# Performance work log

Hardware: AMD Instinct MI355X
Metric: run time of the kernel (lower is better)

Reference implementation:

```python
import jax, jax.numpy as jnp
import numpy as np

N_NODES = 100000
N_EDGES = 3200000

def setup_inputs() -> dict:
    key = jax.random.key(0)
    ks = jax.random.split(key, 13)
    d_in, d1, d2, fm_dims, n_cls = 512, 256, 128, 64, 64
    sc = lambda d: 1.0 / np.sqrt(d)
    return {
        'x': jax.random.normal(ks[0], (N_NODES, d_in), jnp.float32),
        'edge_val': jax.random.uniform(ks[1], (N_EDGES,), jnp.float32),
        'W0': jax.random.normal(ks[2], (d_in, d1), jnp.float32) * sc(d_in),
        'W1': jax.random.normal(ks[3], (d1, d2), jnp.float32) * sc(d1),
        'v0_0': jax.random.normal(ks[4], (d1, 1), jnp.float32) * sc(d1),
        'v0_1': jax.random.normal(ks[5], (d1, 1), jnp.float32) * sc(d1),
        'v1_0': jax.random.normal(ks[6], (d2, 1), jnp.float32) * sc(d2),
        'v1_1': jax.random.normal(ks[7], (d2, 1), jnp.float32) * sc(d2),
        'fm_emb': jax.random.normal(ks[8], (d_in, fm_dims), jnp.float32) * sc(d_in),
        'proj_W': jax.random.normal(ks[9], (d2 + fm_dims, n_cls), jnp.float32) * sc(d2 + fm_dims),
        'proj_b': jnp.zeros((n_cls,), jnp.float32),
        'edge_src': jax.random.randint(ks[10], (N_EDGES,), 0, N_NODES, jnp.int32),
        'edge_dst': jax.random.randint(ks[11], (N_EDGES,), 0, N_NODES, jnp.int32),
    }


def gat_layer(H, W, va, vb, src, dst, a_val, n_nodes):
    # H: [N, d_in] -> Hw: [N, d_out]
    Hw = H @ W
    f1 = (Hw @ va)[:, 0]  # [N]
    f2 = (Hw @ vb)[:, 0]  # [N]
    # per-edge logit: A_ij * f1_i + A_ij * f2_j  (tf sparse broadcast mul + sparse_add)
    logits = a_val * (f1[src] + f2[dst])  # [E]
    s = jax.nn.sigmoid(logits)
    # sparse row softmax over outgoing edges of each src node (stable)
    m = jax.ops.segment_max(s, src, num_segments=n_nodes)  # [N]
    e = jnp.exp(s - m[src])
    denom = jax.ops.segment_sum(e, src, num_segments=n_nodes)  # [N]
    att = e / denom[src]  # [E]
    # aggregate: out[i] = sum_j att_ij * Hw[j]
    out = jax.ops.segment_sum(att[:, None] * Hw[dst], src, num_segments=n_nodes)
    return out


def reference(x, edge_val, W0, W1, v0_0, v0_1, v1_0, v1_1, fm_emb, proj_W, proj_b, edge_src, edge_dst):
    n = x.shape[0]
    # two stacked GAT encoder layers (dropout = 0 at inference)
    H = gat_layer(x, W0, v0_0, v0_1, edge_src, edge_dst, edge_val, n)
    H = gat_layer(H, W1, v1_0, v1_1, edge_src, edge_dst, edge_val, n)
    # NFM bilinear pooling: 0.5 * ((x E)^2 - x (E*E))
    summed = x @ fm_emb
    sq_sum = x @ jnp.square(fm_emb)
    nfm = 0.5 * (jnp.square(summed) - sq_sum)
    # projection to logits
    return jnp.concatenate([H, nfm], axis=1) @ proj_W + proj_b
```

## Files before the change

kernel.cpp:

```cpp
#include <hip/hip_runtime.h>


__device__ __forceinline__ int wave_prefix_incl(int v) {
  int lane = threadIdx.x & 63;
#pragma unroll
  for (int d = 1; d < 64; d <<= 1) {
    int n = __shfl_up(v, d);
    if (lane >= d) v += n;
  }
  return v;
}

__device__ __forceinline__ unsigned short f2bf(float f) {
  unsigned int x = __float_as_uint(f);
  x += 0x7fffu + ((x >> 16) & 1u);
  return (unsigned short)(x >> 16);
}


__global__ void k_hist(const int* __restrict__ src, int* __restrict__ cnt, int E) {
  int e = blockIdx.x * blockDim.x + threadIdx.x;
  if (e < E) atomicAdd(&cnt[src[e]], 1);
}

__global__ void k_scan1(const int* __restrict__ cnt, int* __restrict__ row_ptr,
                        int* __restrict__ partials, int N) {
  int t = threadIdx.x;
  int base = blockIdx.x * 512 + t * 2;
  int e0 = (base < N) ? cnt[base] : 0;
  int e1 = (base + 1 < N) ? cnt[base + 1] : 0;
  int v = e0 + e1;
  int lane = t & 63, wid = t >> 6;
  int incl = wave_prefix_incl(v);
  __shared__ int wsum[4];
  if (lane == 63) wsum[wid] = incl;
  __syncthreads();
  int off = 0;
#pragma unroll
  for (int i = 0; i < 4; ++i)
    if (i < wid) off += wsum[i];
  incl += off;
  int excl = incl - v;
  if (base < N) row_ptr[base] = excl;
  if (base + 1 < N) row_ptr[base + 1] = excl + e0;
  if (t == 255) partials[blockIdx.x] = incl;
}

__global__ void k_scan2(int* partials, int P) {
  int t = threadIdx.x;
  int v = (t < P) ? partials[t] : 0;
  int lane = t & 63, wid = t >> 6;
  int incl = wave_prefix_incl(v);
  __shared__ int wsum[4];
  if (lane == 63) wsum[wid] = incl;
  __syncthreads();
  int off = 0;
#pragma unroll
  for (int i = 0; i < 4; ++i)
    if (i < wid) off += wsum[i];
  incl += off;
  if (t < P) partials[t] = incl - v;
}

__global__ void k_scan3(int* __restrict__ row_ptr, int* __restrict__ cursor,
                        const int* __restrict__ partials, int N, int E) {
  int i = blockIdx.x * blockDim.x + threadIdx.x;
  if (i < N) {
    int v = row_ptr[i] + partials[i >> 9];
    row_ptr[i] = v;
    cursor[i] = v;
  }
  if (i == 0) row_ptr[N] = E;
}

__global__ void k_scatter(const int* __restrict__ src, int* __restrict__ cursor,
                          int* __restrict__ eid, int E) {
  int e = blockIdx.x * blockDim.x + threadIdx.x;
  if (e < E) {
    int p = atomicAdd(&cursor[src[e]], 1);
    eid[p] = e;
  }
}


template <int BM, int BN, int BK>
__global__ __launch_bounds__(256) void k_gemm(const float* __restrict__ A,
                                              const float* __restrict__ B,
                                              float* __restrict__ C, int M, int N,
                                              int K) {
  __shared__ float As[BK][BM];
  __shared__ float Bs[BK][BN];
  int t = threadIdx.x;
  int bm0 = blockIdx.x * BM, bn0 = blockIdx.y * BN;
  int tr = t >> 4, tc = t & 15;
  int row0 = tr * 8, col0 = tc * 4;
  float acc[8][4] = {};
  for (int k0 = 0; k0 < K; k0 += BK) {
#pragma unroll
    for (int i = 0; i < 2; ++i) {
      int s = t + i * 256;
      int ar = s >> 2, akq = (s & 3) * 4;
      int grow = bm0 + ar;
      if (grow >= M) grow = M - 1;
      const float4 av =
          *reinterpret_cast<const float4*>(&A[(size_t)grow * K + k0 + akq]);
      As[akq + 0][ar] = av.x;
      As[akq + 1][ar] = av.y;
      As[akq + 2][ar] = av.z;
      As[akq + 3][ar] = av.w;
    }
    {
      int br = t >> 4, bc = (t & 15) * 4;
      const float4 bv =
          *reinterpret_cast<const float4*>(&B[(size_t)(k0 + br) * N + bn0 + bc]);
      *reinterpret_cast<float4*>(&Bs[br][bc]) = bv;
    }
    __syncthreads();
#pragma unroll
    for (int k = 0; k < BK; ++k) {
      float a0[8], b0[4];
      *reinterpret_cast<float4*>(&a0[0]) =
          *reinterpret_cast<const float4*>(&As[k][row0]);
      *reinterpret_cast<float4*>(&a0[4]) =
          *reinterpret_cast<const float4*>(&As[k][row0 + 4]);
      *reinterpret_cast<float4*>(&b0[0]) =
          *reinterpret_cast<const float4*>(&Bs[k][col0]);
#pragma unroll
      for (int i = 0; i < 8; ++i)
#pragma unroll
        for (int j = 0; j < 4; ++j) acc[i][j] = fmaf(a0[i], b0[j], acc[i][j]);
    }
    __syncthreads();
  }
#pragma unroll
  for (int i = 0; i < 8; ++i) {
    int grow = bm0 + row0 + i;
    if (grow < M) {
      float4 v = {acc[i][0], acc[i][1], acc[i][2], acc[i][3]};
      *reinterpret_cast<float4*>(&C[(size_t)grow * N + bn0 + col0]) = v;
    }
  }
}

template <int BM, int BN, int BK>
__global__ __launch_bounds__(256) void k_gemm_bias(const float* __restrict__ A,
                                                   const float* __restrict__ B,
                                                   const float* __restrict__ bias,
                                                   float* __restrict__ C, int M,
                                                   int N, int K) {
  __shared__ float As[BK][BM];
  __shared__ float Bs[BK][BN];
  int t = threadIdx.x;
  int bm0 = blockIdx.x * BM, bn0 = blockIdx.y * BN;
  int tr = t >> 4, tc = t & 15;
  int row0 = tr * 8, col0 = tc * 4;
  float acc[8][4] = {};
  for (int k0 = 0; k0 < K; k0 += BK) {
#pragma unroll
    for (int i = 0; i < 2; ++i) {
      int s = t + i * 256;
      int ar = s >> 2, akq = (s & 3) * 4;
      int grow = bm0 + ar;
      if (grow >= M) grow = M - 1;
      const float4 av =
          *reinterpret_cast<const float4*>(&A[(size_t)grow * K + k0 + akq]);
      As[akq + 0][ar] = av.x;
      As[akq + 1][ar] = av.y;
      As[akq + 2][ar] = av.z;
      As[akq + 3][ar] = av.w;
    }
    {
      int br = t >> 4, bc = (t & 15) * 4;
      const float4 bv =
          *reinterpret_cast<const float4*>(&B[(size_t)(k0 + br) * N + bn0 + bc]);
      *reinterpret_cast<float4*>(&Bs[br][bc]) = bv;
    }
    __syncthreads();
#pragma unroll
    for (int k = 0; k < BK; ++k) {
      float a0[8], b0[4];
      *reinterpret_cast<float4*>(&a0[0]) =
          *reinterpret_cast<const float4*>(&As[k][row0]);
      *reinterpret_cast<float4*>(&a0[4]) =
          *reinterpret_cast<const float4*>(&As[k][row0 + 4]);
      *reinterpret_cast<float4*>(&b0[0]) =
          *reinterpret_cast<const float4*>(&Bs[k][col0]);
#pragma unroll
      for (int i = 0; i < 8; ++i)
#pragma unroll
        for (int j = 0; j < 4; ++j) acc[i][j] = fmaf(a0[i], b0[j], acc[i][j]);
    }
    __syncthreads();
  }
  const float4 bv = *reinterpret_cast<const float4*>(&bias[bn0 + col0]);
#pragma unroll
  for (int i = 0; i < 8; ++i) {
    int grow = bm0 + row0 + i;
    if (grow < M) {
      float4 v = {acc[i][0] + bv.x, acc[i][1] + bv.y, acc[i][2] + bv.z,
                  acc[i][3] + bv.w};
      *reinterpret_cast<float4*>(&C[(size_t)grow * N + bn0 + col0]) = v;
    }
  }
}

__global__ __launch_bounds__(256) void k_nfm(const float* __restrict__ X,
                                             const float* __restrict__ Emb,
                                             float* __restrict__ out, int M,
                                             int K, int ldo) {
  const int BM = 128, BN = 64, BK = 16;
  __shared__ float As[BK][BM];
  __shared__ float Bs[BK][BN];
  int t = threadIdx.x;
  int bm0 = blockIdx.x * BM;
  int tr = t >> 4, tc = t & 15;
  int row0 = tr * 8, col0 = tc * 4;
  float accS[8][4] = {}, accQ[8][4] = {};
  for (int k0 = 0; k0 < K; k0 += BK) {
#pragma unroll
    for (int i = 0; i < 2; ++i) {
      int s = t + i * 256;
      int ar = s >> 2, akq = (s & 3) * 4;
      int grow = bm0 + ar;
      if (grow >= M) grow = M - 1;
      const float4 av =
          *reinterpret_cast<const float4*>(&X[(size_t)grow * K + k0 + akq]);
      As[akq + 0][ar] = av.x;
      As[akq + 1][ar] = av.y;
      As[akq + 2][ar] = av.z;
      As[akq + 3][ar] = av.w;
    }
    {
      int br = t >> 4, bc = (t & 15) * 4;
      const float4 bv =
          *reinterpret_cast<const float4*>(&Emb[(size_t)(k0 + br) * BN + bc]);
      *reinterpret_cast<float4*>(&Bs[br][bc]) = bv;
    }
    __syncthreads();
#pragma unroll
    for (int k = 0; k < BK; ++k) {
      float a0[8], b0[4], bq[4];
      *reinterpret_cast<float4*>(&a0[0]) =
          *reinterpret_cast<const float4*>(&As[k][row0]);
      *reinterpret_cast<float4*>(&a0[4]) =
          *reinterpret_cast<const float4*>(&As[k][row0 + 4]);
      *reinterpret_cast<float4*>(&b0[0]) =
          *reinterpret_cast<const float4*>(&Bs[k][col0]);
#pragma unroll
      for (int j = 0; j < 4; ++j) bq[j] = b0[j] * b0[j];
#pragma unroll
      for (int i = 0; i < 8; ++i)
#pragma unroll
        for (int j = 0; j < 4; ++j) {
          accS[i][j] = fmaf(a0[i], b0[j], accS[i][j]);
          accQ[i][j] = fmaf(a0[i], bq[j], accQ[i][j]);
        }
    }
    __syncthreads();
  }
#pragma unroll
  for (int i = 0; i < 8; ++i) {
    int grow = bm0 + row0 + i;
    if (grow < M) {
      float4 v;
      v.x = 0.5f * (accS[i][0] * accS[i][0] - accQ[i][0]);
      v.y = 0.5f * (accS[i][1] * accS[i][1] - accQ[i][1]);
      v.z = 0.5f * (accS[i][2] * accS[i][2] - accQ[i][2]);
      v.w = 0.5f * (accS[i][3] * accS[i][3] - accQ[i][3]);
      *reinterpret_cast<float4*>(&out[(size_t)grow * ldo + col0]) = v;
    }
  }
}

__global__ __launch_bounds__(256) void k_cvt_bf16(const float* __restrict__ in,
                                                  unsigned short* __restrict__ out,
                                                  long total) {
  long base = ((long)blockIdx.x * blockDim.x + threadIdx.x) * 8;
  if (base >= total) return;
  float4 a = *reinterpret_cast<const float4*>(&in[base]);
  float4 b = *reinterpret_cast<const float4*>(&in[base + 4]);
  ushort4 lo = {f2bf(a.x), f2bf(a.y), f2bf(a.z), f2bf(a.w)};
  ushort4 hi = {f2bf(b.x), f2bf(b.y), f2bf(b.z), f2bf(b.w)};
  *reinterpret_cast<ushort4*>(&out[base]) = lo;
  *reinterpret_cast<ushort4*>(&out[base + 4]) = hi;
}


template <int D>
__global__ __launch_bounds__(256) void k_fvec(const float* __restrict__ Hw,
                                              const float* __restrict__ va,
                                              const float* __restrict__ vb,
                                              float* __restrict__ f1,
                                              float* __restrict__ f2, int M) {
  int wid = threadIdx.x >> 6, lane = threadIdx.x & 63;
  int i = blockIdx.x * 4 + wid;
  if (i >= M) return;
  const float* row = Hw + (size_t)i * D;
  float s1, s2;
  if (D == 256) {
    float4 h = *reinterpret_cast<const float4*>(&row[lane * 4]);
    float4 a = *reinterpret_cast<const float4*>(&va[lane * 4]);
    float4 b = *reinterpret_cast<const float4*>(&vb[lane * 4]);
    s1 = h.x * a.x + h.y * a.y + h.z * a.z + h.w * a.w;
    s2 = h.x * b.x + h.y * b.y + h.z * b.z + h.w * b.w;
  } else {
    float2 h = *reinterpret_cast<const float2*>(&row[lane * 2]);
    float2 a = *reinterpret_cast<const float2*>(&va[lane * 2]);
    float2 b = *reinterpret_cast<const float2*>(&vb[lane * 2]);
    s1 = h.x * a.x + h.y * a.y;
    s2 = h.x * b.x + h.y * b.y;
  }
#pragma unroll
  for (int d = 32; d; d >>= 1) {
    s1 += __shfl_down(s1, d);
    s2 += __shfl_down(s2, d);
  }
  if (lane == 0) {
    f1[i] = s1;
    f2[i] = s2;
  }
}

__global__ void k_edge(const float* __restrict__ aval, const int* __restrict__ src,
                       const int* __restrict__ dst, const float* __restrict__ f1,
                       const float* __restrict__ f2, float* __restrict__ att,
                       float* __restrict__ denom, int E) {
  int e = blockIdx.x * blockDim.x + threadIdx.x;
  if (e >= E) return;
  float x = aval[e] * (f1[src[e]] + f2[dst[e]]);
  float s = 1.0f / (1.0f + __expf(-x));
  float ev = __expf(s);
  att[e] = ev;
  atomicAdd(&denom[src[e]], ev);
}

template <int D>
__global__ __launch_bounds__(256) void k_agg(const unsigned short* __restrict__ Hwb,
                                             const float* __restrict__ att,
                                             const int* __restrict__ row_ptr,
                                             const int* __restrict__ eid,
                                             const int* __restrict__ dst,
                                             const float* __restrict__ denom,
                                             float* __restrict__ out, int M,
                                             int ldo) {
  int wid = threadIdx.x >> 6, lane = threadIdx.x & 63;
  int i = blockIdx.x * 4 + wid;
  if (i >= M) return;
  int p0 = __builtin_amdgcn_readfirstlane(row_ptr[i]);
  int p1 = __builtin_amdgcn_readfirstlane(row_ptr[i + 1]);
  float acc[8] = {};
  if (D == 256) {
    int half = lane >> 5, q = lane & 31;
    for (int p = p0 + half; p < p1; p += 2) {
      int e = eid[p];
      float w = att[e];
      int j = dst[e];
      uint4 hv =
          *reinterpret_cast<const uint4*>(&Hwb[(size_t)j * 256 + q * 8]);
#pragma unroll
      for (int c = 0; c < 4; ++c) {
        unsigned int u = (&hv.x)[c];
        acc[2 * c + 0] = fmaf(w, __uint_as_float(u << 16), acc[2 * c + 0]);
        acc[2 * c + 1] = fmaf(w, __uint_as_float(u & 0xffff0000u), acc[2 * c + 1]);
      }
    }
#pragma unroll
    for (int c = 0; c < 8; ++c) acc[c] += __shfl_xor(acc[c], 32);
    if (half == 0) {
      float inv = (p1 > p0) ? 1.0f / denom[i] : 0.0f;
      float4 lo = {acc[0] * inv, acc[1] * inv, acc[2] * inv, acc[3] * inv};
      float4 hi = {acc[4] * inv, acc[5] * inv, acc[6] * inv, acc[7] * inv};
      *reinterpret_cast<float4*>(&out[(size_t)i * ldo + q * 8]) = lo;
      *reinterpret_cast<float4*>(&out[(size_t)i * ldo + q * 8 + 4]) = hi;
    }
  } else {
    int quarter = lane >> 4, q = lane & 15;
    for (int p = p0 + quarter; p < p1; p += 4) {
      int e = eid[p];
      float w = att[e];
      int j = dst[e];
      uint4 hv =
          *reinterpret_cast<const uint4*>(&Hwb[(size_t)j * 128 + q * 8]);
#pragma unroll
      for (int c = 0; c < 4; ++c) {
        unsigned int u = (&hv.x)[c];
        acc[2 * c + 0] = fmaf(w, __uint_as_float(u << 16), acc[2 * c + 0]);
        acc[2 * c + 1] = fmaf(w, __uint_as_float(u & 0xffff0000u), acc[2 * c + 1]);
      }
    }
#pragma unroll
    for (int c = 0; c < 8; ++c) acc[c] += __shfl_xor(acc[c], 32);
#pragma unroll
    for (int c = 0; c < 8; ++c) acc[c] += __shfl_xor(acc[c], 16);
    if (quarter == 0) {
      float inv = (p1 > p0) ? 1.0f / denom[i] : 0.0f;
      float4 lo = {acc[0] * inv, acc[1] * inv, acc[2] * inv, acc[3] * inv};
      float4 hi = {acc[4] * inv, acc[5] * inv, acc[6] * inv, acc[7] * inv};
      *reinterpret_cast<float4*>(&out[(size_t)i * ldo + q * 8]) = lo;
      *reinterpret_cast<float4*>(&out[(size_t)i * ldo + q * 8 + 4]) = hi;
    }
  }
}


extern "C" void kernel_launch(void* const* d_in, const int* in_sizes, int n_in,
                              void* d_out, int out_size, void* d_ws, size_t ws_size,
                              hipStream_t stream) {
  (void)n_in;
  (void)out_size;
  const float* x = (const float*)d_in[0];
  const float* aval = (const float*)d_in[1];
  const float* W0 = (const float*)d_in[2];
  const float* W1 = (const float*)d_in[3];
  const float* v00 = (const float*)d_in[4];
  const float* v01 = (const float*)d_in[5];
  const float* v10 = (const float*)d_in[6];
  const float* v11 = (const float*)d_in[7];
  const float* fme = (const float*)d_in[8];
  const float* pW = (const float*)d_in[9];
  const float* pb = (const float*)d_in[10];
  const int* esrc = (const int*)d_in[11];
  const int* edst = (const int*)d_in[12];
  const int N = in_sizes[0] / 512;
  const int E = in_sizes[1];
  float* out = (float*)d_out;

  char* w = (char*)d_ws;
  size_t off = 0;
  auto alloc = [&](size_t bytes) -> char* {
    char* p = w + off;
    off += (bytes + 255) & ~(size_t)255;
    return p;
  };
  float* bufA = (float*)alloc((size_t)N * 256 * 4);
  unsigned short* bufB = (unsigned short*)alloc((size_t)N * 256 * 2);
  float* bufC = (float*)alloc((size_t)N * 128 * 4);
  float* f1 = (float*)alloc((size_t)N * 4);
  float* f2 = (float*)alloc((size_t)N * 4);
  float* dnm = (float*)alloc((size_t)N * 4);
  float* att = (float*)alloc((size_t)E * 4);
  int* cnt = (int*)alloc((size_t)N * 4);
  int* rp = (int*)alloc((size_t)(N + 1) * 4);
  int* cur = (int*)alloc((size_t)N * 4);
  int* eid = (int*)alloc((size_t)E * 4);
  int* part = (int*)alloc(4096);
  if (off > ws_size) return;

  float* Hw0 = bufA;
  unsigned short* Hwb0 = bufB;
  float* H1 = bufA;
  float* Hw1 = bufC;
  unsigned short* Hwb1 = bufB;
  float* Hcat = bufA;

  const int TPB = 256;
  int egrid = (E + TPB - 1) / TPB;
  int ngrid4 = (N + 3) / 4;
  int P = (N + 511) / 512;

  hipMemsetAsync(cnt, 0, (size_t)N * 4, stream);
  k_hist<<<egrid, TPB, 0, stream>>>(esrc, cnt, E);
  k_scan1<<<P, TPB, 0, stream>>>(cnt, rp, part, N);
  k_scan2<<<1, TPB, 0, stream>>>(part, P);
  k_scan3<<<(N + TPB) / TPB, TPB, 0, stream>>>(rp, cur, part, N, E);
  k_scatter<<<egrid, TPB, 0, stream>>>(esrc, cur, eid, E);

  {
    dim3 g((N + 127) / 128, 256 / 64);
    k_gemm<128, 64, 16><<<g, TPB, 0, stream>>>(x, W0, Hw0, N, 256, 512);
  }
  k_fvec<256><<<ngrid4, TPB, 0, stream>>>(Hw0, v00, v01, f1, f2, N);
  {
    long total = (long)N * 256;
    int g = (int)((total / 8 + TPB - 1) / TPB);
    k_cvt_bf16<<<g, TPB, 0, stream>>>(Hw0, Hwb0, total);
  }
  hipMemsetAsync(dnm, 0, (size_t)N * 4, stream);
  k_edge<<<egrid, TPB, 0, stream>>>(aval, esrc, edst, f1, f2, att, dnm, E);
  k_agg<256><<<ngrid4, TPB, 0, stream>>>(Hwb0, att, rp, eid, edst, dnm, H1, N, 256);

  {
    dim3 g((N + 127) / 128, 128 / 64);
    k_gemm<128, 64, 16><<<g, TPB, 0, stream>>>(H1, W1, Hw1, N, 128, 256);
  }
  k_nfm<<<(N + 127) / 128, TPB, 0, stream>>>(x, fme, Hcat + 128, N, 512, 192);
  k_fvec<128><<<ngrid4, TPB, 0, stream>>>(Hw1, v10, v11, f1, f2, N);
  {
    long total = (long)N * 128;
    int g = (int)((total / 8 + TPB - 1) / TPB);
    k_cvt_bf16<<<g, TPB, 0, stream>>>(Hw1, Hwb1, total);
  }
  hipMemsetAsync(dnm, 0, (size_t)N * 4, stream);
  k_edge<<<egrid, TPB, 0, stream>>>(aval, esrc, edst, f1, f2, att, dnm, E);
  k_agg<128><<<ngrid4, TPB, 0, stream>>>(Hwb1, att, rp, eid, edst, dnm, Hcat, N, 192);

  {
    dim3 g((N + 127) / 128, 1);
    k_gemm_bias<128, 64, 16><<<g, TPB, 0, stream>>>(Hcat, pW, pb, out, N, 64, 192);
  }
}
```

Before: 2.328 ms.

## Fuse bf16 conversion and attention score dot products into GEMM epilogue

The GEMM epilogue now writes Hw directly as bf16 and computes the f1/f2 attention projections with a 16-lane shuffle reduction plus atomicAdd per column tile. This removes the separate fp32 Hw write, the k_cvt_bf16 and k_fvec kernels and their re-reads of Hw. It also pads the shared-memory tiles by 4 floats in all GEMM kernels to reduce LDS bank conflicts. In exchange it adds extra memsets for f1/f2 and atomics across column blocks, which makes the f1/f2 summation order non-deterministic.

```diff
diff --git a/kernel.cpp b/kernel.cpp
--- a/kernel.cpp
+++ b/kernel.cpp
@@ -82,14 +82,14 @@
   }
 }
 
-
 template <int BM, int BN, int BK>
-__global__ __launch_bounds__(256) void k_gemm(const float* __restrict__ A,
-                                              const float* __restrict__ B,
-                                              float* __restrict__ C, int M, int N,
-                                              int K) {
-  __shared__ float As[BK][BM];
-  __shared__ float Bs[BK][BN];
+__global__ __launch_bounds__(256) void k_gemm_bf16_fv(
+    const float* __restrict__ A, const float* __restrict__ B,
+    const float* __restrict__ va, const float* __restrict__ vb,
+    unsigned short* __restrict__ Cb, float* __restrict__ f1,
+    float* __restrict__ f2, int M, int N, int K) {
+  __shared__ float As[BK][BM + 4];
+  __shared__ float Bs[BK][BN + 4];
   int t = threadIdx.x;
   int bm0 = blockIdx.x * BM, bn0 = blockIdx.y * BN;
   int tr = t >> 4, tc = t & 15;
@@ -132,12 +132,29 @@
     }
     __syncthreads();
   }
+  const float4 va4 = *reinterpret_cast<const float4*>(&va[bn0 + col0]);
+  const float4 vb4 = *reinterpret_cast<const float4*>(&vb[bn0 + col0]);
 #pragma unroll
   for (int i = 0; i < 8; ++i) {
     int grow = bm0 + row0 + i;
-    if (grow < M) {
-      float4 v = {acc[i][0], acc[i][1], acc[i][2], acc[i][3]};
-      *reinterpret_cast<float4*>(&C[(size_t)grow * N + bn0 + col0]) = v;
+    bool live = grow < M;
+    if (live) {
+      ushort4 o = {f2bf(acc[i][0]), f2bf(acc[i][1]), f2bf(acc[i][2]),
+                   f2bf(acc[i][3])};
+      *reinterpret_cast<ushort4*>(&Cb[(size_t)grow * N + bn0 + col0]) = o;
+    }
+    float p1 = acc[i][0] * va4.x + acc[i][1] * va4.y + acc[i][2] * va4.z +
+               acc[i][3] * va4.w;
+    float p2 = acc[i][0] * vb4.x + acc[i][1] * vb4.y + acc[i][2] * vb4.z +
+               acc[i][3] * vb4.w;
+#pragma unroll
+    for (int d = 1; d < 16; d <<= 1) {
+      p1 += __shfl_xor(p1, d);
+      p2 += __shfl_xor(p2, d);
+    }
+    if (live && tc == 0) {
+      atomicAdd(&f1[grow], p1);
+      atomicAdd(&f2[grow], p2);
     }
   }
 }
@@ -148,8 +165,8 @@
                                                    const float* __restrict__ bias,
                                                    float* __restrict__ C, int M,
                                                    int N, int K) {
-  __shared__ float As[BK][BM];
-  __shared__ float Bs[BK][BN];
+  __shared__ float As[BK][BM + 4];
+  __shared__ float Bs[BK][BN + 4];
   int t = threadIdx.x;
   int bm0 = blockIdx.x * BM, bn0 = blockIdx.y * BN;
   int tr = t >> 4, tc = t & 15;
@@ -209,8 +226,8 @@
                                              float* __restrict__ out, int M,
                                              int K, int ldo) {
   const int BM = 128, BN = 64, BK = 16;
-  __shared__ float As[BK][BM];
-  __shared__ float Bs[BK][BN];
+  __shared__ float As[BK][BM + 4];
+  __shared__ float Bs[BK][BN + 4];
   int t = threadIdx.x;
   int bm0 = blockIdx.x * BM;
   int tr = t >> 4, tc = t & 15;
@@ -272,54 +289,6 @@
   }
 }
 
-__global__ __launch_bounds__(256) void k_cvt_bf16(const float* __restrict__ in,
-                                                  unsigned short* __restrict__ out,
-                                                  long total) {
-  long base = ((long)blockIdx.x * blockDim.x + threadIdx.x) * 8;
-  if (base >= total) return;
-  float4 a = *reinterpret_cast<const float4*>(&in[base]);
-  float4 b = *reinterpret_cast<const float4*>(&in[base + 4]);
-  ushort4 lo = {f2bf(a.x), f2bf(a.y), f2bf(a.z), f2bf(a.w)};
-  ushort4 hi = {f2bf(b.x), f2bf(b.y), f2bf(b.z), f2bf(b.w)};
-  *reinterpret_cast<ushort4*>(&out[base]) = lo;
-  *reinterpret_cast<ushort4*>(&out[base + 4]) = hi;
-}
-
-
-template <int D>
-__global__ __launch_bounds__(256) void k_fvec(const float* __restrict__ Hw,
-                                              const float* __restrict__ va,
-                                              const float* __restrict__ vb,
-                                              float* __restrict__ f1,
-                                              float* __restrict__ f2, int M) {
-  int wid = threadIdx.x >> 6, lane = threadIdx.x & 63;
-  int i = blockIdx.x * 4 + wid;
-  if (i >= M) return;
-  const float* row = Hw + (size_t)i * D;
-  float s1, s2;
-  if (D == 256) {
-    float4 h = *reinterpret_cast<const float4*>(&row[lane * 4]);
-    float4 a = *reinterpret_cast<const float4*>(&va[lane * 4]);
-    float4 b = *reinterpret_cast<const float4*>(&vb[lane * 4]);
-    s1 = h.x * a.x + h.y * a.y + h.z * a.z + h.w * a.w;
-    s2 = h.x * b.x + h.y * b.y + h.z * b.z + h.w * b.w;
-  } else {
-    float2 h = *reinterpret_cast<const float2*>(&row[lane * 2]);
-    float2 a = *reinterpret_cast<const float2*>(&va[lane * 2]);
-    float2 b = *reinterpret_cast<const float2*>(&vb[lane * 2]);
-    s1 = h.x * a.x + h.y * a.y;
-    s2 = h.x * b.x + h.y * b.y;
-  }
-#pragma unroll
-  for (int d = 32; d; d >>= 1) {
-    s1 += __shfl_down(s1, d);
-    s2 += __shfl_down(s2, d);
-  }
-  if (lane == 0) {
-    f1[i] = s1;
-    f2[i] = s2;
-  }
-}
 
 __global__ void k_edge(const float* __restrict__ aval, const int* __restrict__ src,
                        const int* __restrict__ dst, const float* __restrict__ f1,
@@ -434,7 +403,6 @@
   };
   float* bufA = (float*)alloc((size_t)N * 256 * 4);
   unsigned short* bufB = (unsigned short*)alloc((size_t)N * 256 * 2);
-  float* bufC = (float*)alloc((size_t)N * 128 * 4);
   float* f1 = (float*)alloc((size_t)N * 4);
   float* f2 = (float*)alloc((size_t)N * 4);
   float* dnm = (float*)alloc((size_t)N * 4);
@@ -446,10 +414,8 @@
   int* part = (int*)alloc(4096);
   if (off > ws_size) return;
 
-  float* Hw0 = bufA;
   unsigned short* Hwb0 = bufB;
   float* H1 = bufA;
-  float* Hw1 = bufC;
   unsigned short* Hwb1 = bufB;
   float* Hcat = bufA;
 
@@ -465,32 +431,26 @@
   k_scan3<<<(N + TPB) / TPB, TPB, 0, stream>>>(rp, cur, part, N, E);
   k_scatter<<<egrid, TPB, 0, stream>>>(esrc, cur, eid, E);
 
+  hipMemsetAsync(f1, 0, (size_t)N * 4, stream);
+  hipMemsetAsync(f2, 0, (size_t)N * 4, stream);
+  hipMemsetAsync(dnm, 0, (size_t)N * 4, stream);
   {
     dim3 g((N + 127) / 128, 256 / 64);
-    k_gemm<128, 64, 16><<<g, TPB, 0, stream>>>(x, W0, Hw0, N, 256, 512);
-  }
-  k_fvec<256><<<ngrid4, TPB, 0, stream>>>(Hw0, v00, v01, f1, f2, N);
-  {
-    long total = (long)N * 256;
-    int g = (int)((total / 8 + TPB - 1) / TPB);
-    k_cvt_bf16<<<g, TPB, 0, stream>>>(Hw0, Hwb0, total);
-  }
-  hipMemsetAsync(dnm, 0, (size_t)N * 4, stream);
+    k_gemm_bf16_fv<128, 64, 16>
+        <<<g, TPB, 0, stream>>>(x, W0, v00, v01, Hwb0, f1, f2, N, 256, 512);
+  }
   k_edge<<<egrid, TPB, 0, stream>>>(aval, esrc, edst, f1, f2, att, dnm, E);
   k_agg<256><<<ngrid4, TPB, 0, stream>>>(Hwb0, att, rp, eid, edst, dnm, H1, N, 256);
 
+  hipMemsetAsync(f1, 0, (size_t)N * 4, stream);
+  hipMemsetAsync(f2, 0, (size_t)N * 4, stream);
+  hipMemsetAsync(dnm, 0, (size_t)N * 4, stream);
   {
     dim3 g((N + 127) / 128, 128 / 64);
-    k_gemm<128, 64, 16><<<g, TPB, 0, stream>>>(H1, W1, Hw1, N, 128, 256);
+    k_gemm_bf16_fv<128, 64, 16>
+        <<<g, TPB, 0, stream>>>(H1, W1, v10, v11, Hwb1, f1, f2, N, 128, 256);
   }
   k_nfm<<<(N + 127) / 128, TPB, 0, stream>>>(x, fme, Hcat + 128, N, 512, 192);
-  k_fvec<128><<<ngrid4, TPB, 0, stream>>>(Hw1, v10, v11, f1, f2, N);
-  {
-    long total = (long)N * 128;
-    int g = (int)((total / 8 + TPB - 1) / TPB);
-    k_cvt_bf16<<<g, TPB, 0, stream>>>(Hw1, Hwb1, total);
-  }
-  hipMemsetAsync(dnm, 0, (size_t)N * 4, stream);
   k_edge<<<egrid, TPB, 0, stream>>>(aval, esrc, edst, f1, f2, att, dnm, E);
   k_agg<128><<<ngrid4, TPB, 0, stream>>>(Hwb1, att, rp, eid, edst, dnm, Hcat, N, 192);
 
```

New measurement: 2.221 ms. 1.05x faster.
